# Kernel optimization log

Measured on AMD Instinct MI355X. Metric: run time of the kernel, lower is better.

The kernel has to match this reference:

```python
import jax, jax.numpy as jnp
import numpy as np

B, S, D, H = 2, 2048, 1024, 16
DK = D // H  # 64


def rotate_half(x):
    d = x.shape[-1]
    x1, x2 = x[..., : d // 2], x[..., d // 2 :]
    return jnp.concatenate([-x2, x1], axis=-1)


def apply_rope(q, k):
    # q, k: [B, H, S, DK]
    d_k = q.shape[-1]
    seq_len = q.shape[-2]
    theta = 10000.0 ** (-2.0 / d_k * jnp.arange(d_k // 2, dtype=q.dtype))
    positions = jnp.arange(seq_len, dtype=q.dtype)
    angles = jnp.outer(positions, theta)                    # [S, DK/2]
    cos = jnp.tile(jnp.cos(angles), (1, 2))                 # [S, DK]
    sin = jnp.tile(jnp.sin(angles), (1, 2))
    q = q * cos + rotate_half(q) * sin
    k = k * cos + rotate_half(k) * sin
    return q, k


def setup_inputs() -> dict:
    key = jax.random.key(0)
    ks = jax.random.split(key, 9)
    std = 1.0 / np.sqrt(D)
    x = jax.random.normal(ks[0], (B, S, D), dtype=jnp.float32)
    # mask True = masked (code uses masked_fill(mask, -inf)); causal mask
    mask = jnp.triu(jnp.ones((S, S), dtype=bool), k=1)[None, None, :, :]
    mask = jnp.broadcast_to(mask, (B, 1, S, S))
    Wq = jax.random.uniform(ks[1], (D, D), jnp.float32, -std, std)
    bq = jax.random.uniform(ks[2], (D,), jnp.float32, -std, std)
    Wk = jax.random.uniform(ks[3], (D, D), jnp.float32, -std, std)
    bk = jax.random.uniform(ks[4], (D,), jnp.float32, -std, std)
    Wv = jax.random.uniform(ks[5], (D, D), jnp.float32, -std, std)
    bv = jax.random.uniform(ks[6], (D,), jnp.float32, -std, std)
    Wo = jax.random.uniform(ks[7], (D, D), jnp.float32, -std, std)
    bo = jax.random.uniform(ks[8], (D,), jnp.float32, -std, std)
    return {"x": x, "mask": mask, "Wq": Wq, "bq": bq, "Wk": Wk, "bk": bk,
            "Wv": Wv, "bv": bv, "Wo": Wo, "bo": bo}


def reference(x, mask, Wq, bq, Wk, bk, Wv, bv, Wo, bo):
    b, s, d = x.shape
    # projections -> [B, H, S, DK]
    q = (x @ Wq + bq).reshape(b, s, H, DK).transpose(0, 2, 1, 3)
    k = (x @ Wk + bk).reshape(b, s, H, DK).transpose(0, 2, 1, 3)
    v = (x @ Wv + bv).reshape(b, s, H, DK).transpose(0, 2, 1, 3)
    q, k = apply_rope(q, k)
    scores = jnp.einsum("bhqd,bhkd->bhqk", q, k) / np.sqrt(DK)
    scores = jnp.where(mask, -jnp.inf, scores)
    probs = jax.nn.softmax(scores, axis=-1)
    attn = jnp.einsum("bhqk,bhkd->bhqd", probs, v)
    o = attn.transpose(0, 2, 1, 3).reshape(b, s, H * DK)
    return o @ Wo + bo
```

## Files before the change

### kernel.cpp

```cpp
#include <hip/hip_runtime.h>
#include <hip/hip_bf16.h>
#include <math.h>

typedef __hip_bfloat16 bf16;
typedef __attribute__((ext_vector_type(8))) short short8;
typedef __attribute__((ext_vector_type(4))) short s16x4;
typedef __attribute__((ext_vector_type(4))) float f32x4;

#define B_  2
#define S_  2048
#define D_  1024
#define H_  16
#define DK_ 64

#define QSCALE 0.18033688011112043f
#define EXPOFF 11.541560327111707f

__device__ inline short bfs(float f) { return __builtin_bit_cast(short, __float2bfloat16(f)); }

#define GLL16(gptr, lptr)                                                        \
    __builtin_amdgcn_global_load_lds(                                            \
        (const __attribute__((address_space(1))) void*)(gptr),                   \
        (__attribute__((address_space(3))) void*)(lptr), 16, 0, 0)

#if __has_builtin(__builtin_amdgcn_mfma_f32_16x16x16bf16_1k)
#define MFMA_16x16x16(A, Bv, C) __builtin_amdgcn_mfma_f32_16x16x16bf16_1k(A, Bv, C, 0, 0, 0)
#elif __has_builtin(__builtin_amdgcn_mfma_f32_16x16x16_bf16)
#define MFMA_16x16x16(A, Bv, C) __builtin_amdgcn_mfma_f32_16x16x16_bf16(A, Bv, C, 0, 0, 0)
#else
static __device__ inline f32x4 mfma16_asm(s16x4 a, s16x4 b, f32x4 c) {
    f32x4 d;
    asm volatile("v_mfma_f32_16x16x16_bf16 %0, %1, %2, %3\n\ts_nop 7\n\ts_nop 7"
                 : "=v"(d) : "v"(a), "v"(b), "v"(c));
    return d;
}
#define MFMA_16x16x16(A, Bv, C) mfma16_asm(A, Bv, C)
#endif

__global__ __launch_bounds__(256)
void prep_k(const float* __restrict__ x,
            const float* __restrict__ W0, const float* __restrict__ W1,
            const float* __restrict__ W2, const float* __restrict__ W3,
            bf16* __restrict__ cx, bf16* __restrict__ Wt)
{
    const int z = blockIdx.z;
    const int t = threadIdx.x;
    if (z == 4) {
        const int bid = blockIdx.y * 16 + blockIdx.x;
        #pragma unroll
        for (int i = 0; i < 16; i++) {
            const size_t g = ((size_t)bid * 256 + t) * 4 + (size_t)i * 262144;
            const float4 v = *(const float4*)(x + g);
            s16x4 o = { bfs(v.x), bfs(v.y), bfs(v.z), bfs(v.w) };
            *(s16x4*)(cx + g) = o;
        }
        return;
    }
    __shared__ float Lt[64][65];
    const float* W = (z == 0) ? W0 : (z == 1) ? W1 : (z == 2) ? W2 : W3;
    bf16* dst = Wt + (size_t)z * D_ * D_;
    const int k0 = blockIdx.y * 64, n0 = blockIdx.x * 64;
    #pragma unroll
    for (int p = 0; p < 4; p++) {
        const int idx = p * 256 + t;
        const int row = idx >> 4, cb = (idx & 15) * 4;
        const float4 v = *(const float4*)(W + (size_t)(k0 + row) * D_ + n0 + cb);
        Lt[cb + 0][row] = v.x; Lt[cb + 1][row] = v.y;
        Lt[cb + 2][row] = v.z; Lt[cb + 3][row] = v.w;
    }
    __syncthreads();
    #pragma unroll
    for (int p = 0; p < 4; p++) {
        const int idx = p * 256 + t;
        const int n = idx >> 4, kb = (idx & 15) * 4;
        s16x4 o = { bfs(Lt[n][kb]), bfs(Lt[n][kb + 1]), bfs(Lt[n][kb + 2]), bfs(Lt[n][kb + 3]) };
        *(s16x4*)(dst + (size_t)(n0 + n) * D_ + k0 + kb) = o;
    }
}

template<int MODE, int TM>
__global__ __launch_bounds__(256)
void gemm_k(const bf16* __restrict__ A, const bf16* __restrict__ WtAll,
            const float* __restrict__ b0, const float* __restrict__ b1,
            const float* __restrict__ b2,
            bf16* __restrict__ d0, bf16* __restrict__ d1, bf16* __restrict__ d2,
            float* __restrict__ fout)
{
    constexpr int K = D_;
    constexpr int MT = (B_ * S_) / TM;
    constexpr int AI = TM / 64;
    const int L = (int)blockIdx.x;
    const int m0 = (L & (MT - 1)) * TM;
    const int rest = L / MT;
    const int z = (MODE == 0) ? (rest >> 4) : 3;
    const int n0 = (MODE == 0) ? (rest & 15) * 64 : rest * 64;
    const bf16* W = WtAll + (size_t)z * D_ * D_;
    const float* bias = (MODE == 1) ? b0 : ((z == 0) ? b0 : (z == 1) ? b1 : b2);

    __shared__ __align__(16) short As[TM * 32];
    __shared__ __align__(16) short Bs[64 * 32];

    const int t = threadIdx.x;
    const int wave = t >> 6, lane = t & 63, quad = lane >> 4, l16 = lane & 15;
    const int wm = wave * (TM / 4);

    const bf16* gA0 = A + (size_t)(m0 + (t >> 2)) * K + (t & 3) * 8;
    const bf16* gA1 = gA0 + (size_t)64 * K;
    const bf16* gW0 = W + (size_t)(n0 + (t >> 2)) * K + (t & 3) * 8;
    const int wb = wave * 512;

    f32x4 acc[AI][4] = {};

    for (int k0 = 0; k0 < K; k0 += 32) {
        __syncthreads();
        GLL16(gA0 + k0, &As[wb]);
        if (TM == 128) GLL16(gA1 + k0, &As[2048 + wb]);
        GLL16(gW0 + k0, &Bs[wb]);
        __syncthreads();
        short8 af[AI], bfv[4];
        #pragma unroll
        for (int i = 0; i < AI; i++) af[i] = *(const short8*)&As[(wm + i * 16 + l16) * 32 + quad * 8];
        #pragma unroll
        for (int j = 0; j < 4; j++) bfv[j] = *(const short8*)&Bs[(j * 16 + l16) * 32 + quad * 8];
        #pragma unroll
        for (int i = 0; i < AI; i++)
            #pragma unroll
            for (int j = 0; j < 4; j++)
                acc[i][j] = __builtin_amdgcn_mfma_f32_16x16x32_bf16(af[i], bfv[j], acc[i][j], 0, 0, 0);
    }

    if (MODE == 1) {
        #pragma unroll
        for (int j = 0; j < 4; j++) {
            const int ncol = n0 + j * 16 + l16;
            const float bb = bias[ncol];
            #pragma unroll
            for (int i = 0; i < AI; i++) {
                const int mbase = m0 + wm + i * 16 + quad * 4;
                #pragma unroll
                for (int r = 0; r < 4; r++)
                    fout[(size_t)(mbase + r) * D_ + ncol] = acc[i][j][r] + bb;
            }
        }
    } else if (z == 2) {
        const int h = n0 >> 6;
        #pragma unroll
        for (int j = 0; j < 4; j++) {
            const int ncol = n0 + j * 16 + l16;
            const float bb = bias[ncol];
            const int dk = ncol & 63;
            #pragma unroll
            for (int i = 0; i < AI; i++) {
                const int mbase = m0 + wm + i * 16 + quad * 4;
                #pragma unroll
                for (int r = 0; r < 4; r++) {
                    const int m = mbase + r;
                    const int b = m >> 11, s = m & (S_ - 1);
                    d2[(((size_t)(b * H_ + h)) * DK_ + dk) * S_ + s] = __float2bfloat16(acc[i][j][r] + bb);
                }
            }
        }
    } else {
        bf16* dst = z ? d1 : d0;
        const float sc = z ? 1.0f : QSCALE;
        const int h = n0 >> 6;
        #pragma unroll
        for (int j = 0; j < 2; j++) {
            const int dk = j * 16 + l16;
            const float th = exp2f((float)dk * -0.41524101186092029f);
            const float blo = bias[(h << 6) + dk];
            const float bhi = bias[(h << 6) + dk + 32];
            #pragma unroll
            for (int i = 0; i < AI; i++) {
                #pragma unroll
                for (int r = 0; r < 4; r++) {
                    const int m = m0 + wm + i * 16 + quad * 4 + r;
                    const int b = m >> 11, s = m & (S_ - 1);
                    float sn, cs;
                    sincosf((float)s * th, &sn, &cs);
                    const float v1 = acc[i][j][r] + blo;
                    const float v2 = acc[i][j + 2][r] + bhi;
                    bf16* p = dst + (((size_t)(b * H_ + h)) * S_ + s) * DK_;
                    p[dk]      = __float2bfloat16((v1 * cs - v2 * sn) * sc);
                    p[dk + 32] = __float2bfloat16((v2 * cs + v1 * sn) * sc);
                }
            }
        }
    }
}

__global__ __launch_bounds__(256)
void gemm_o(const bf16* __restrict__ A, const bf16* __restrict__ Wt3,
            const float* __restrict__ bias, float* __restrict__ fout)
{
    constexpr int K = D_;
    const int L = (int)blockIdx.x;
    const int m0 = (L & 63) * 64;
    const int n0 = (L >> 6) * 64;

    __shared__ __align__(16) short As[64 * 64];
    __shared__ __align__(16) short Bs[64 * 64];

    const int t = threadIdx.x;
    const int wave = t >> 6, lane = t & 63, quad = lane >> 4, l16 = lane & 15;
    const int wm = wave * 16;

    const int srow  = t >> 3;
    const int sslot = (t & 7) ^ (srow & 7);
    const bf16* gA = A   + (size_t)(m0 + srow) * K + sslot * 8;
    const bf16* gW = Wt3 + (size_t)(n0 + srow) * K + sslot * 8;
    const int wb = wave * 512;

    f32x4 acc[4] = {};

    for (int k0 = 0; k0 < K; k0 += 64) {
        __syncthreads();
        GLL16(gA + k0,                  &As[wb]);
        GLL16(gA + k0 + (size_t)32 * K, &As[2048 + wb]);
        GLL16(gW + k0,                  &Bs[wb]);
        GLL16(gW + k0 + (size_t)32 * K, &Bs[2048 + wb]);
        __syncthreads();

        const int swz = l16 & 7;
        short8 af[2], bfv[4][2];
        #pragma unroll
        for (int c = 0; c < 2; c++) {
            af[c] = *(const short8*)&As[(wm + l16) * 64 + ((c * 4 + quad) ^ swz) * 8];
            #pragma unroll
            for (int j = 0; j < 4; j++)
                bfv[j][c] = *(const short8*)&Bs[(j * 16 + l16) * 64 + ((c * 4 + quad) ^ swz) * 8];
        }
        #pragma unroll
        for (int c = 0; c < 2; c++)
            #pragma unroll
            for (int j = 0; j < 4; j++)
                acc[j] = __builtin_amdgcn_mfma_f32_16x16x32_bf16(af[c], bfv[j][c], acc[j], 0, 0, 0);
    }

    #pragma unroll
    for (int j = 0; j < 4; j++) {
        const int ncol = n0 + j * 16 + l16;
        const float bb = bias[ncol];
        const int mbase = m0 + wm + quad * 4;
        #pragma unroll
        for (int r = 0; r < 4; r++)
            fout[(size_t)(mbase + r) * D_ + ncol] = acc[j][r] + bb;
    }
}

template<bool DIAG>
__device__ __forceinline__
void attn_tile(const short* __restrict__ Ks, const short* __restrict__ Vts,
               const short8 qf0, const short8 qf1,
               f32x4* ot, float& l_acc,
               const int wave, const int quad, const int l16)
{
    const int kkmax = DIAG ? wave : 3;
    #pragma unroll
    for (int kk = 0; kk <= kkmax; kk++) {
        const short8 kf0 = *(const short8*)&Ks[(kk * 16 + l16) * 72 + quad * 8];
        const short8 kf1 = *(const short8*)&Ks[(kk * 16 + l16) * 72 + 32 + quad * 8];
        f32x4 st = {};
        st = __builtin_amdgcn_mfma_f32_16x16x32_bf16(kf0, qf0, st, 0, 0, 0);
        st = __builtin_amdgcn_mfma_f32_16x16x32_bf16(kf1, qf1, st, 0, 0, 0);

        s16x4 pt;
        float psum = 0.0f;
        #pragma unroll
        for (int r = 0; r < 4; r++) {
            float p;
            if (DIAG) {
                const bool masked = (kk == wave) && (quad * 4 + r > l16);
                p = masked ? 0.0f : exp2f(st[r] - EXPOFF);
            } else {
                p = exp2f(st[r] - EXPOFF);
            }
            psum += p;
            pt[r] = bfs(p);
        }
        l_acc += psum;

        #pragma unroll
        for (int dt = 0; dt < 4; dt++) {
            const s16x4 vf = *(const s16x4*)&Vts[(dt * 16 + l16) * 72 + kk * 16 + quad * 4];
            ot[dt] = MFMA_16x16x16(vf, pt, ot[dt]);
        }
    }
}

__global__ __launch_bounds__(256)
void attn_k(const bf16* __restrict__ q_ws, const bf16* __restrict__ k_ws,
            const bf16* __restrict__ vt_ws, bf16* __restrict__ attn_ws)
{
    __shared__ __align__(16) short Ks[64 * 72];
    __shared__ __align__(16) short Vts[64 * 72];

    const int bh = (int)blockIdx.x;
    const int by = (int)blockIdx.y;
    const int j8 = by & 7, g = by >> 3;
    const int qt = (g == 0) ? (31 - j8) : (g == 1) ? j8 : (g == 2) ? (23 - j8) : (8 + j8);

    const int t = threadIdx.x;
    const int wave = t >> 6, quad = (t & 63) >> 4, l16 = t & 15;
    const bf16* Kb = k_ws + (size_t)bh * S_ * DK_;
    const bf16* Vb = vt_ws + (size_t)bh * DK_ * S_;
    const int b = bh >> 4, h = bh & 15;

    const bf16* Qb = q_ws + ((size_t)bh * S_ + qt * 64 + wave * 16) * DK_;
    const short8 qf0 = *(const short8*)(Qb + (size_t)l16 * DK_ + quad * 8);
    const short8 qf1 = *(const short8*)(Qb + (size_t)l16 * DK_ + 32 + quad * 8);

    float l_acc = 0.0f;
    f32x4 ot[4] = {};

    for (int kt = 0; kt <= qt; kt++) {
        __syncthreads();
        #pragma unroll
        for (int p = 0; p < 2; p++) {
            const int idx = p * 256 + t;
            const int row = idx >> 3, cb = (idx & 7) * 8;
            *(float4*)&Ks[row * 72 + cb]  = *(const float4*)(Kb + (size_t)(kt * 64 + row) * DK_ + cb);
            *(float4*)&Vts[row * 72 + cb] = *(const float4*)(Vb + (size_t)row * S_ + kt * 64 + cb);
        }
        __syncthreads();

        if (kt == qt) attn_tile<true >(Ks, Vts, qf0, qf1, ot, l_acc, wave, quad, l16);
        else          attn_tile<false>(Ks, Vts, qf0, qf1, ot, l_acc, wave, quad, l16);
    }

    l_acc += __shfl_xor(l_acc, 16, 64);
    l_acc += __shfl_xor(l_acc, 32, 64);
    const float inv = 1.0f / l_acc;
    const int srow = qt * 64 + wave * 16 + l16;
    bf16* orow = attn_ws + ((size_t)(b * S_ + srow)) * D_ + h * 64;
    #pragma unroll
    for (int dt = 0; dt < 4; dt++) {
        s16x4 o4 = { bfs(ot[dt][0] * inv), bfs(ot[dt][1] * inv),
                     bfs(ot[dt][2] * inv), bfs(ot[dt][3] * inv) };
        *(s16x4*)(orow + dt * 16 + quad * 4) = o4;
    }
}

extern "C" void kernel_launch(void* const* d_in, const int* in_sizes, int n_in,
                              void* d_out, int out_size, void* d_ws, size_t ws_size,
                              hipStream_t stream)
{
    (void)out_size; (void)ws_size;
    const float* x = nullptr;
    const float* W[4] = {nullptr, nullptr, nullptr, nullptr};
    const float* bias[4] = {nullptr, nullptr, nullptr, nullptr};
    int wi = 0, bi = 0;
    for (int i = 0; i < n_in; i++) {
        const int sz = in_sizes[i];
        if (sz == B_ * S_ * D_ && x == nullptr) x = (const float*)d_in[i];
        else if (sz == D_ * D_ && wi < 4) W[wi++] = (const float*)d_in[i];
        else if (sz == D_ && bi < 4) bias[bi++] = (const float*)d_in[i];
    }

    bf16* ws = (bf16*)d_ws;
    const size_t SEG = (size_t)B_ * S_ * D_;
    bf16* canonX  = ws;
    bf16* Wt      = ws + SEG;
    bf16* k_ws    = ws + 2 * SEG;
    bf16* vt_ws   = ws + 3 * SEG;
    bf16* attn_ws = canonX;
    bf16* q_ws    = (bf16*)d_out;

    prep_k<<<dim3(16, 16, 5), 256, 0, stream>>>(x, W[0], W[1], W[2], W[3], canonX, Wt);

    gemm_k<0, 128><<<dim3(1536, 1, 1), 256, 0, stream>>>(
        canonX, Wt, bias[0], bias[1], bias[2], q_ws, k_ws, vt_ws, nullptr);

    attn_k<<<dim3(32, 32), 256, 0, stream>>>(q_ws, k_ws, vt_ws, attn_ws);

    gemm_o<<<dim3(1024, 1, 1), 256, 0, stream>>>(
        attn_ws, Wt + (size_t)3 * D_ * D_, bias[3], (float*)d_out);
}
```

Measured before the change: 214.9 us.

## Widen QKV GEMM K-tile to 64 with swizzled LDS and precompute RoPE table

The QKV projection GEMM now stages 64-wide K slices into XOR-swizzled shared memory. This halves the number of barrier pairs per K loop and is meant to avoid LDS bank conflicts on fragment reads. The RoPE cos/sin values are computed once per (position, dim) into a table by an extra prep block slice, replacing per-element sincosf in the GEMM epilogue with a table load. The table lives in the second half of the output buffer, which relies on that space being free until the final GEMM writes it.

```diff
diff --git a/kernel.cpp b/kernel.cpp
--- a/kernel.cpp
+++ b/kernel.cpp
@@ -41,7 +41,8 @@
 void prep_k(const float* __restrict__ x,
             const float* __restrict__ W0, const float* __restrict__ W1,
             const float* __restrict__ W2, const float* __restrict__ W3,
-            bf16* __restrict__ cx, bf16* __restrict__ Wt)
+            bf16* __restrict__ cx, bf16* __restrict__ Wt,
+            float2* __restrict__ rope)
 {
     const int z = blockIdx.z;
     const int t = threadIdx.x;
@@ -54,6 +55,16 @@
             s16x4 o = { bfs(v.x), bfs(v.y), bfs(v.z), bfs(v.w) };
             *(s16x4*)(cx + g) = o;
         }
+        return;
+    }
+    if (z == 5) {
+        const int bid = blockIdx.y * 16 + blockIdx.x;
+        const int idx = bid * 256 + t;
+        const int s = idx >> 5, dk = idx & 31;
+        const float th = exp2f((float)dk * -0.41524101186092029f);
+        float sn, cs;
+        sincosf((float)s * th, &sn, &cs);
+        rope[idx] = make_float2(cs, sn);
         return;
     }
     __shared__ float Lt[64][65];
@@ -78,71 +89,64 @@
     }
 }
 
-template<int MODE, int TM>
 __global__ __launch_bounds__(256)
-void gemm_k(const bf16* __restrict__ A, const bf16* __restrict__ WtAll,
-            const float* __restrict__ b0, const float* __restrict__ b1,
-            const float* __restrict__ b2,
-            bf16* __restrict__ d0, bf16* __restrict__ d1, bf16* __restrict__ d2,
-            float* __restrict__ fout)
+void gemm_qkv(const bf16* __restrict__ A, const bf16* __restrict__ WtAll,
+              const float* __restrict__ b0, const float* __restrict__ b1,
+              const float* __restrict__ b2, const float2* __restrict__ rope,
+              bf16* __restrict__ d0, bf16* __restrict__ d1, bf16* __restrict__ d2)
 {
     constexpr int K = D_;
-    constexpr int MT = (B_ * S_) / TM;
-    constexpr int AI = TM / 64;
     const int L = (int)blockIdx.x;
-    const int m0 = (L & (MT - 1)) * TM;
-    const int rest = L / MT;
-    const int z = (MODE == 0) ? (rest >> 4) : 3;
-    const int n0 = (MODE == 0) ? (rest & 15) * 64 : rest * 64;
+    const int m0 = (L & 31) * 128;
+    const int rest = L >> 5;
+    const int z = rest >> 4;
+    const int n0 = (rest & 15) * 64;
     const bf16* W = WtAll + (size_t)z * D_ * D_;
-    const float* bias = (MODE == 1) ? b0 : ((z == 0) ? b0 : (z == 1) ? b1 : b2);
-
-    __shared__ __align__(16) short As[TM * 32];
-    __shared__ __align__(16) short Bs[64 * 32];
+    const float* bias = (z == 0) ? b0 : (z == 1) ? b1 : b2;
+
+    __shared__ __align__(16) short As[128 * 64];
+    __shared__ __align__(16) short Bs[64 * 64];
 
     const int t = threadIdx.x;
     const int wave = t >> 6, lane = t & 63, quad = lane >> 4, l16 = lane & 15;
-    const int wm = wave * (TM / 4);
-
-    const bf16* gA0 = A + (size_t)(m0 + (t >> 2)) * K + (t & 3) * 8;
-    const bf16* gA1 = gA0 + (size_t)64 * K;
-    const bf16* gW0 = W + (size_t)(n0 + (t >> 2)) * K + (t & 3) * 8;
+    const int wm = wave * 32;
+
+    const int srow  = t >> 3;
+    const int sslot = (t & 7) ^ (srow & 7);
+    const bf16* gA = A + (size_t)(m0 + srow) * K + sslot * 8;
+    const bf16* gW = W + (size_t)(n0 + srow) * K + sslot * 8;
     const int wb = wave * 512;
 
-    f32x4 acc[AI][4] = {};
-
-    for (int k0 = 0; k0 < K; k0 += 32) {
-        __syncthreads();
-        GLL16(gA0 + k0, &As[wb]);
-        if (TM == 128) GLL16(gA1 + k0, &As[2048 + wb]);
-        GLL16(gW0 + k0, &Bs[wb]);
-        __syncthreads();
-        short8 af[AI], bfv[4];
-        #pragma unroll
-        for (int i = 0; i < AI; i++) af[i] = *(const short8*)&As[(wm + i * 16 + l16) * 32 + quad * 8];
-        #pragma unroll
-        for (int j = 0; j < 4; j++) bfv[j] = *(const short8*)&Bs[(j * 16 + l16) * 32 + quad * 8];
-        #pragma unroll
-        for (int i = 0; i < AI; i++)
-            #pragma unroll
-            for (int j = 0; j < 4; j++)
-                acc[i][j] = __builtin_amdgcn_mfma_f32_16x16x32_bf16(af[i], bfv[j], acc[i][j], 0, 0, 0);
-    }
-
-    if (MODE == 1) {
-        #pragma unroll
-        for (int j = 0; j < 4; j++) {
-            const int ncol = n0 + j * 16 + l16;
-            const float bb = bias[ncol];
-            #pragma unroll
-            for (int i = 0; i < AI; i++) {
-                const int mbase = m0 + wm + i * 16 + quad * 4;
+    f32x4 acc[2][4] = {};
+
+    for (int k0 = 0; k0 < K; k0 += 64) {
+        __syncthreads();
+        GLL16(gA + k0,                  &As[wb]);
+        GLL16(gA + k0 + (size_t)32 * K, &As[2048 + wb]);
+        GLL16(gA + k0 + (size_t)64 * K, &As[4096 + wb]);
+        GLL16(gA + k0 + (size_t)96 * K, &As[6144 + wb]);
+        GLL16(gW + k0,                  &Bs[wb]);
+        GLL16(gW + k0 + (size_t)32 * K, &Bs[2048 + wb]);
+        __syncthreads();
+
+        const int swz = l16 & 7;
+        #pragma unroll
+        for (int c = 0; c < 2; c++) {
+            const int slot = ((c * 4 + quad) ^ swz) * 8;
+            short8 af[2], bfv[4];
+            #pragma unroll
+            for (int i = 0; i < 2; i++) af[i] = *(const short8*)&As[(wm + i * 16 + l16) * 64 + slot];
+            #pragma unroll
+            for (int j = 0; j < 4; j++) bfv[j] = *(const short8*)&Bs[(j * 16 + l16) * 64 + slot];
+            #pragma unroll
+            for (int i = 0; i < 2; i++)
                 #pragma unroll
-                for (int r = 0; r < 4; r++)
-                    fout[(size_t)(mbase + r) * D_ + ncol] = acc[i][j][r] + bb;
-            }
-        }
-    } else if (z == 2) {
+                for (int j = 0; j < 4; j++)
+                    acc[i][j] = __builtin_amdgcn_mfma_f32_16x16x32_bf16(af[i], bfv[j], acc[i][j], 0, 0, 0);
+        }
+    }
+
+    if (z == 2) {
         const int h = n0 >> 6;
         #pragma unroll
         for (int j = 0; j < 4; j++) {
@@ -150,7 +154,7 @@
             const float bb = bias[ncol];
             const int dk = ncol & 63;
             #pragma unroll
-            for (int i = 0; i < AI; i++) {
+            for (int i = 0; i < 2; i++) {
                 const int mbase = m0 + wm + i * 16 + quad * 4;
                 #pragma unroll
                 for (int r = 0; r < 4; r++) {
@@ -167,22 +171,20 @@
         #pragma unroll
         for (int j = 0; j < 2; j++) {
             const int dk = j * 16 + l16;
-            const float th = exp2f((float)dk * -0.41524101186092029f);
             const float blo = bias[(h << 6) + dk];
             const float bhi = bias[(h << 6) + dk + 32];
             #pragma unroll
-            for (int i = 0; i < AI; i++) {
+            for (int i = 0; i < 2; i++) {
                 #pragma unroll
                 for (int r = 0; r < 4; r++) {
                     const int m = m0 + wm + i * 16 + quad * 4 + r;
                     const int b = m >> 11, s = m & (S_ - 1);
-                    float sn, cs;
-                    sincosf((float)s * th, &sn, &cs);
+                    const float2 cc = rope[(s << 5) + dk];
                     const float v1 = acc[i][j][r] + blo;
                     const float v2 = acc[i][j + 2][r] + bhi;
                     bf16* p = dst + (((size_t)(b * H_ + h)) * S_ + s) * DK_;
-                    p[dk]      = __float2bfloat16((v1 * cs - v2 * sn) * sc);
-                    p[dk + 32] = __float2bfloat16((v2 * cs + v1 * sn) * sc);
+                    p[dk]      = __float2bfloat16((v1 * cc.x - v2 * cc.y) * sc);
+                    p[dk + 32] = __float2bfloat16((v2 * cc.x + v1 * cc.y) * sc);
                 }
             }
         }
@@ -365,11 +367,12 @@
     bf16* vt_ws   = ws + 3 * SEG;
     bf16* attn_ws = canonX;
     bf16* q_ws    = (bf16*)d_out;
-
-    prep_k<<<dim3(16, 16, 5), 256, 0, stream>>>(x, W[0], W[1], W[2], W[3], canonX, Wt);
-
-    gemm_k<0, 128><<<dim3(1536, 1, 1), 256, 0, stream>>>(
-        canonX, Wt, bias[0], bias[1], bias[2], q_ws, k_ws, vt_ws, nullptr);
+    float2* rope  = (float2*)((bf16*)d_out + SEG);
+
+    prep_k<<<dim3(16, 16, 6), 256, 0, stream>>>(x, W[0], W[1], W[2], W[3], canonX, Wt, rope);
+
+    gemm_qkv<<<dim3(1536, 1, 1), 256, 0, stream>>>(
+        canonX, Wt, bias[0], bias[1], bias[2], rope, q_ws, k_ws, vt_ws);
 
     attn_k<<<dim3(32, 32), 256, 0, stream>>>(q_ws, k_ws, vt_ws, attn_ws);
 
```

Measured after the change: 203.1 us. 5.5% less time.
